# Performance work log

Hardware: AMD Instinct MI355X
Metric: run time of the kernel (lower is better)

Reference implementation:

```python
import jax, jax.numpy as jnp
import numpy as np
import math

B, S, D, H, DFF, L = 8, 1024, 512, 8, 2048, 4
DK = D // H
EPS = 1e-5
NEG = -1e32


def _sinusoidal_pe(s, d):
    pos = np.arange(s)[:, None].astype(np.float32)
    div = np.exp(np.arange(0, d, 2).astype(np.float32) * (-math.log(10000.0) / d))
    pe = np.zeros((s, d), np.float32)
    pe[:, 0::2] = np.sin(pos * div)
    pe[:, 1::2] = np.cos(pos * div)
    return jnp.asarray(pe)


def setup_inputs() -> dict:
    key = jax.random.key(0)
    ks = jax.random.split(key, 20)
    sd = 0.02
    inp = {
        "q_embed_data": jax.random.normal(ks[0], (B, S, D), jnp.float32),
        "qa_embed_data": jax.random.normal(ks[1], (B, S, D), jnp.float32),
        "pe": _sinusoidal_pe(S, D),
        # stacked per-layer params (leading dim L). kq_same=1 -> q uses Wk.
        "Wk": sd * jax.random.normal(ks[2], (L, D, D), jnp.float32),
        "bk": jnp.zeros((L, D), jnp.float32),
        "Wv": sd * jax.random.normal(ks[3], (L, D, D), jnp.float32),
        "bv": jnp.zeros((L, D), jnp.float32),
        "Wo": sd * jax.random.normal(ks[4], (L, D, D), jnp.float32),
        "bo": jnp.zeros((L, D), jnp.float32),
        "ln1_s": jnp.ones((L, D), jnp.float32),
        "ln1_b": jnp.zeros((L, D), jnp.float32),
        "W1": sd * jax.random.normal(ks[5], (L, D, DFF), jnp.float32),
        "b1": jnp.zeros((L, DFF), jnp.float32),
        "W2": sd * jax.random.normal(ks[6], (L, DFF, D), jnp.float32),
        "b2": jnp.zeros((L, D), jnp.float32),
        "ln2_s": jnp.ones((L, D), jnp.float32),
        "ln2_b": jnp.zeros((L, D), jnp.float32),
    }
    return inp


def _layernorm(z, s, b):
    m = z.mean(-1, keepdims=True)
    v = ((z - m) ** 2).mean(-1, keepdims=True)
    return (z - m) / jnp.sqrt(v + EPS) * s + b


def _forward(q_embed_data, qa_embed_data, pe, Wk, bk, Wv, bv, Wo, bo,
             ln1_s, ln1_b, W1, b1, W2, b2, ln2_s, ln2_b):
    x = q_embed_data + pe[None, :, :]
    y = qa_embed_data + pe[None, :, :]  # values source stays fixed across blocks
    allowed = jnp.tril(jnp.ones((S, S), bool), -1)  # strictly-causal: attend only to j < i
    row_keep = (jnp.arange(S) > 0).astype(x.dtype)[None, None, :, None]  # zero_pad row 0

    def heads(z, W, b):
        return (z @ W + b).reshape(B, S, H, DK).transpose(0, 2, 1, 3)  # [B,H,S,DK]

    def step(xc, p):
        wk, bk_, wv, bv_, wo, bo_, s1, b1n, w1, b1f, w2, b2f, s2, b2n = p
        q = heads(xc, wk, bk_)  # kq_same: q via k_linear
        k = heads(xc, wk, bk_)
        v = heads(y, wv, bv_)
        sc = jnp.einsum('bhid,bhjd->bhij', q, k) / math.sqrt(DK)
        att = jax.nn.softmax(jnp.where(allowed, sc, NEG), axis=-1) * row_keep
        o = jnp.einsum('bhij,bhjd->bhid', att, v).transpose(0, 2, 1, 3).reshape(B, S, D)
        x1 = _layernorm(xc + (o @ wo + bo_), s1, b1n)
        f = jax.nn.relu(x1 @ w1 + b1f) @ w2 + b2f
        x2 = _layernorm(x1 + f, s2, b2n)
        return x2, None

    out, _ = jax.lax.scan(step, x, (Wk, bk, Wv, bv, Wo, bo, ln1_s, ln1_b, W1, b1, W2, b2, ln2_s, ln2_b))
    return out


def reference(q_embed_data, qa_embed_data, pe, Wk, bk, Wv, bv, Wo, bo,
              ln1_s, ln1_b, W1, b1, W2, b2, ln2_s, ln2_b):
    return _forward(q_embed_data, qa_embed_data, pe, Wk, bk, Wv, bv, Wo, bo,
                    ln1_s, ln1_b, W1, b1, W2, b2, ln2_s, ln2_b)
```

## Files before the change

kernel.cpp:

```cpp
#include <hip/hip_runtime.h>
#include <stdint.h>

typedef __attribute__((ext_vector_type(8))) __bf16 bf16x8;
typedef __attribute__((ext_vector_type(4))) float f32x4;
typedef __attribute__((ext_vector_type(4))) unsigned int u32x4;

constexpr int B = 8, S = 1024, D = 512, H = 8, DFF = 2048, L = 4, DK = 64;
constexpr int MR = B * S;

__device__ __forceinline__ unsigned short f2bf(float f) {
    union { float f; unsigned u; } v; v.f = f;
    unsigned u = v.u;
    u += 0x7fffu + ((u >> 16) & 1u);
    return (unsigned short)(u >> 16);
}

__device__ __forceinline__ void gload_lds16(const void* g, void* l) {
    __builtin_amdgcn_global_load_lds(
        (const __attribute__((address_space(1))) void*)g,
        (__attribute__((address_space(3))) void*)l, 16, 0, 0);
}

__global__ __launch_bounds__(256) void add_pe_kernel(
    const float* __restrict__ qe, const float* __restrict__ qa,
    const float* __restrict__ pe, float* __restrict__ x_f32,
    unsigned short* __restrict__ x_bf, unsigned short* __restrict__ y_bf) {
    int gid = blockIdx.x * 256 + threadIdx.x;
    int base = gid * 4;
    int po = base & (S * D - 1);
    float4 p = *(const float4*)(pe + po);
    float4 a = *(const float4*)(qe + base);
    float4 q = *(const float4*)(qa + base);
    float4 xv = make_float4(a.x + p.x, a.y + p.y, a.z + p.z, a.w + p.w);
    float4 yv = make_float4(q.x + p.x, q.y + p.y, q.z + p.z, q.w + p.w);
    *(float4*)(x_f32 + base) = xv;
    ushort4 xb; xb.x = f2bf(xv.x); xb.y = f2bf(xv.y); xb.z = f2bf(xv.z); xb.w = f2bf(xv.w);
    ushort4 yb; yb.x = f2bf(yv.x); yb.y = f2bf(yv.y); yb.z = f2bf(yv.z); yb.w = f2bf(yv.w);
    *(ushort4*)(x_bf + base) = xb;
    *(ushort4*)(y_bf + base) = yb;
}

__global__ __launch_bounds__(256) void wtrans_kernel(
    const float* __restrict__ src, unsigned short* __restrict__ dst, int K, int N) {
    __shared__ float t[64][65];
    src += (size_t)blockIdx.z * K * N;
    dst += (size_t)blockIdx.z * K * N;
    int n0 = blockIdx.x * 64, k0 = blockIdx.y * 64;
    int tid = threadIdx.x;
    int r = tid >> 4, c4 = (tid & 15) * 4;
    #pragma unroll
    for (int rr = 0; rr < 64; rr += 16) {
        float4 v = *(const float4*)(src + (size_t)(k0 + r + rr) * N + n0 + c4);
        t[r + rr][c4] = v.x; t[r + rr][c4 + 1] = v.y;
        t[r + rr][c4 + 2] = v.z; t[r + rr][c4 + 3] = v.w;
    }
    __syncthreads();
    int n = tid >> 2, kc = (tid & 3) * 16;
    ushort4 o[4];
    #pragma unroll
    for (int g = 0; g < 4; g++) {
        o[g].x = f2bf(t[kc + g * 4 + 0][n]);
        o[g].y = f2bf(t[kc + g * 4 + 1][n]);
        o[g].z = f2bf(t[kc + g * 4 + 2][n]);
        o[g].w = f2bf(t[kc + g * 4 + 3][n]);
    }
    unsigned short* dp = dst + (size_t)(n0 + n) * K + k0 + kc;
    #pragma unroll
    for (int g = 0; g < 4; g++) *(ushort4*)(dp + g * 4) = o[g];
}

template<int BN, bool RELU, bool RESID, bool OUT_F32, bool OUT_BF16, bool OUT_VT>
__global__ __launch_bounds__(256) void gemm_kernel(
    const unsigned short* __restrict__ A, const unsigned short* __restrict__ Bt,
    const float* __restrict__ bias, const float* __restrict__ resid,
    float* __restrict__ out_f32, unsigned short* __restrict__ out_bf,
    int M, int N, int K) {
    constexpr int MT = (BN == 128) ? 4 : 2;
    constexpr int WROWS = (BN == 128) ? 64 : 32;
    constexpr int BRND = (BN == 128) ? 4 : 2;
    __shared__ unsigned short a_lds[128 * 64];
    __shared__ unsigned short b_lds[BN * 64];

    const int tid = threadIdx.x;
    const int lane = tid & 63, wid = tid >> 6;
    const int wm = (BN == 128) ? (wid >> 1) : wid;
    const int wn = (BN == 128) ? (wid & 1) : 0;
    const int l15 = lane & 15, quad = lane >> 4;
    const int nmt = gridDim.x, nnt = gridDim.y;
    const int o_lin = blockIdx.y * nmt + blockIdx.x;
    const int xcd = o_lin & 7, oi = o_lin >> 3;
    const int mtile = xcd * (nmt >> 3) + oi / nnt;
    const int ntile = oi % nnt;
    const int m0 = mtile * 128, n0 = ntile * BN;

    f32x4 acc[MT][4];
    #pragma unroll
    for (int i = 0; i < MT; i++)
        #pragma unroll
        for (int j = 0; j < 4; j++) { f32x4 z = {0.f, 0.f, 0.f, 0.f}; acc[i][j] = z; }

    const unsigned short* aP[4];
    unsigned short* aL[4];
    #pragma unroll
    for (int j = 0; j < 4; j++) {
        int c = wid * 256 + j * 64 + lane;
        int r = c >> 3, slot = c & 7, kg = slot ^ (r & 7);
        aP[j] = A + (size_t)(m0 + r) * K + kg * 8;
        aL[j] = a_lds + (size_t)(wid * 256 + j * 64) * 8;
    }
    const unsigned short* bP[BRND];
    unsigned short* bL[BRND];
    #pragma unroll
    for (int j = 0; j < BRND; j++) {
        int c = wid * (BRND * 64) + j * 64 + lane;
        int r = c >> 3, slot = c & 7, kg = slot ^ (r & 7);
        bP[j] = Bt + (size_t)(n0 + r) * K + kg * 8;
        bL[j] = b_lds + (size_t)(wid * (BRND * 64) + j * 64) * 8;
    }

    for (int k0 = 0; k0 < K; k0 += 64) {
        #pragma unroll
        for (int j = 0; j < 4; j++) gload_lds16(aP[j] + k0, aL[j]);
        #pragma unroll
        for (int j = 0; j < BRND; j++) gload_lds16(bP[j] + k0, bL[j]);
        __syncthreads();

        bf16x8 af[MT][2], bfv[4][2];
        #pragma unroll
        for (int mt = 0; mt < MT; mt++) {
            int row = wm * WROWS + mt * 16 + l15;
            #pragma unroll
            for (int kh = 0; kh < 2; kh++)
                af[mt][kh] = *(const bf16x8*)&a_lds[row * 64 + (((kh * 4 + quad) ^ (row & 7)) * 8)];
        }
        #pragma unroll
        for (int nt = 0; nt < 4; nt++) {
            int row = wn * 64 + nt * 16 + l15;
            #pragma unroll
            for (int kh = 0; kh < 2; kh++)
                bfv[nt][kh] = *(const bf16x8*)&b_lds[row * 64 + (((kh * 4 + quad) ^ (row & 7)) * 8)];
        }
        #pragma unroll
        for (int mt = 0; mt < MT; mt++)
            #pragma unroll
            for (int nt = 0; nt < 4; nt++) {
                acc[mt][nt] = __builtin_amdgcn_mfma_f32_16x16x32_bf16(af[mt][0], bfv[nt][0], acc[mt][nt], 0, 0, 0);
                acc[mt][nt] = __builtin_amdgcn_mfma_f32_16x16x32_bf16(af[mt][1], bfv[nt][1], acc[mt][nt], 0, 0, 0);
            }
        __syncthreads();
    }

    #pragma unroll
    for (int nt = 0; nt < 4; nt++) {
        int col = n0 + wn * 64 + nt * 16 + l15;
        float bv = bias[col];
        #pragma unroll
        for (int mt = 0; mt < MT; mt++) {
            int row0 = m0 + wm * WROWS + mt * 16 + quad * 4;
            if (OUT_VT) {
                int hh = col >> 6, d = col & 63;
                int bb = row0 >> 10, s0 = row0 & 1023;
                ushort4 o;
                o.x = f2bf(acc[mt][nt][0] + bv);
                o.y = f2bf(acc[mt][nt][1] + bv);
                o.z = f2bf(acc[mt][nt][2] + bv);
                o.w = f2bf(acc[mt][nt][3] + bv);
                *(ushort4*)(out_bf + ((size_t)(bb * H + hh) * DK + d) * S + s0) = o;
            } else {
                #pragma unroll
                for (int r = 0; r < 4; r++) {
                    int row = row0 + r;
                    float v = acc[mt][nt][r] + bv;
                    if (RESID) v += resid[(size_t)row * N + col];
                    if (RELU) v = fmaxf(v, 0.f);
                    size_t o = (size_t)row * N + col;
                    if (OUT_F32) out_f32[o] = v;
                    if (OUT_BF16) out_bf[o] = f2bf(v);
                }
            }
        }
    }
}

__global__ __launch_bounds__(256) void gemm_qkv_kernel(
    const unsigned short* __restrict__ x_bf, const unsigned short* __restrict__ y_bf,
    const unsigned short* __restrict__ wkT, const unsigned short* __restrict__ wvT,
    const float* __restrict__ bk, const float* __restrict__ bv,
    unsigned short* __restrict__ qk_out, unsigned short* __restrict__ vt_out) {
    constexpr int BN = 64, MT = 2, WROWS = 32, BRND = 2;
    constexpr int N = 512, K = 512;
    __shared__ unsigned short a_lds[128 * 64];
    __shared__ unsigned short b_lds[BN * 64];

    const bool isv = blockIdx.z != 0;
    const unsigned short* A  = isv ? y_bf : x_bf;
    const unsigned short* Bt = isv ? wvT : wkT;
    const float* bias        = isv ? bv : bk;

    const int tid = threadIdx.x;
    const int lane = tid & 63, wid = tid >> 6;
    const int l15 = lane & 15, quad = lane >> 4;
    const int nmt = gridDim.x, nnt = gridDim.y;
    const int o_lin = blockIdx.y * nmt + blockIdx.x;
    const int xcd = o_lin & 7, oi = o_lin >> 3;
    const int mtile = xcd * (nmt >> 3) + oi / nnt;
    const int ntile = oi % nnt;
    const int m0 = mtile * 128, n0 = ntile * BN;

    f32x4 acc[MT][4];
    #pragma unroll
    for (int i = 0; i < MT; i++)
        #pragma unroll
        for (int j = 0; j < 4; j++) { f32x4 z = {0.f, 0.f, 0.f, 0.f}; acc[i][j] = z; }

    const unsigned short* aP[4];
    unsigned short* aL[4];
    #pragma unroll
    for (int j = 0; j < 4; j++) {
        int c = wid * 256 + j * 64 + lane;
        int r = c >> 3, slot = c & 7, kg = slot ^ (r & 7);
        aP[j] = A + (size_t)(m0 + r) * K + kg * 8;
        aL[j] = a_lds + (size_t)(wid * 256 + j * 64) * 8;
    }
    const unsigned short* bP[BRND];
    unsigned short* bL[BRND];
    #pragma unroll
    for (int j = 0; j < BRND; j++) {
        int c = wid * (BRND * 64) + j * 64 + lane;
        int r = c >> 3, slot = c & 7, kg = slot ^ (r & 7);
        bP[j] = Bt + (size_t)(n0 + r) * K + kg * 8;
        bL[j] = b_lds + (size_t)(wid * (BRND * 64) + j * 64) * 8;
    }

    for (int k0 = 0; k0 < K; k0 += 64) {
        #pragma unroll
        for (int j = 0; j < 4; j++) gload_lds16(aP[j] + k0, aL[j]);
        #pragma unroll
        for (int j = 0; j < BRND; j++) gload_lds16(bP[j] + k0, bL[j]);
        __syncthreads();

        bf16x8 af[MT][2], bfv[4][2];
        #pragma unroll
        for (int mt = 0; mt < MT; mt++) {
            int row = wid * WROWS + mt * 16 + l15;
            #pragma unroll
            for (int kh = 0; kh < 2; kh++)
                af[mt][kh] = *(const bf16x8*)&a_lds[row * 64 + (((kh * 4 + quad) ^ (row & 7)) * 8)];
        }
        #pragma unroll
        for (int nt = 0; nt < 4; nt++) {
            int row = nt * 16 + l15;
            #pragma unroll
            for (int kh = 0; kh < 2; kh++)
                bfv[nt][kh] = *(const bf16x8*)&b_lds[row * 64 + (((kh * 4 + quad) ^ (row & 7)) * 8)];
        }
        #pragma unroll
        for (int mt = 0; mt < MT; mt++)
            #pragma unroll
            for (int nt = 0; nt < 4; nt++) {
                acc[mt][nt] = __builtin_amdgcn_mfma_f32_16x16x32_bf16(af[mt][0], bfv[nt][0], acc[mt][nt], 0, 0, 0);
                acc[mt][nt] = __builtin_amdgcn_mfma_f32_16x16x32_bf16(af[mt][1], bfv[nt][1], acc[mt][nt], 0, 0, 0);
            }
        __syncthreads();
    }

    #pragma unroll
    for (int nt = 0; nt < 4; nt++) {
        int col = n0 + nt * 16 + l15;
        float bv_ = bias[col];
        #pragma unroll
        for (int mt = 0; mt < MT; mt++) {
            int row0 = m0 + wid * WROWS + mt * 16 + quad * 4;
            ushort4 o;
            o.x = f2bf(acc[mt][nt][0] + bv_);
            o.y = f2bf(acc[mt][nt][1] + bv_);
            o.z = f2bf(acc[mt][nt][2] + bv_);
            o.w = f2bf(acc[mt][nt][3] + bv_);
            if (isv) {
                int hh = col >> 6, d = col & 63;
                int bb = row0 >> 10, s0 = row0 & 1023;
                *(ushort4*)(vt_out + ((size_t)(bb * H + hh) * DK + d) * S + s0) = o;
            } else {
                #pragma unroll
                for (int r = 0; r < 4; r++)
                    qk_out[(size_t)(row0 + r) * N + col] =
                        (r == 0) ? o.x : (r == 1) ? o.y : (r == 2) ? o.z : o.w;
            }
        }
    }
}

__global__ __launch_bounds__(256) void ln_kernel(
    const float* __restrict__ in, const float* __restrict__ gamma,
    const float* __restrict__ beta, float* __restrict__ out_f32,
    unsigned short* __restrict__ out_bf) {
    __shared__ float red[8];
    int row = blockIdx.x, tid = threadIdx.x;
    const float* p = in + (size_t)row * D;
    float2 v = *(const float2*)(p + tid * 2);
    float s = v.x + v.y;
    float q = v.x * v.x + v.y * v.y;
    #pragma unroll
    for (int off = 32; off > 0; off >>= 1) {
        s += __shfl_xor(s, off);
        q += __shfl_xor(q, off);
    }
    int wid = tid >> 6, lane = tid & 63;
    if (lane == 0) { red[wid] = s; red[4 + wid] = q; }
    __syncthreads();
    s = red[0] + red[1] + red[2] + red[3];
    q = red[4] + red[5] + red[6] + red[7];
    float mean = s * (1.f / D);
    float var = q * (1.f / D) - mean * mean;
    float inv = rsqrtf(var + 1e-5f);
    int c = tid * 2;
    float2 g = *(const float2*)(gamma + c);
    float2 bb = *(const float2*)(beta + c);
    float o0 = (v.x - mean) * inv * g.x + bb.x;
    float o1 = (v.y - mean) * inv * g.y + bb.y;
    *(float2*)(out_f32 + (size_t)row * D + c) = make_float2(o0, o1);
    ushort2 ob; ob.x = f2bf(o0); ob.y = f2bf(o1);
    *(ushort2*)(out_bf + (size_t)row * D + c) = ob;
}

__global__ __launch_bounds__(256, 2) void attn_kernel(
    const unsigned short* __restrict__ qk, const unsigned short* __restrict__ vt,
    unsigned short* __restrict__ ob) {
    __shared__ unsigned short kbuf[2][64 * 64];
    __shared__ unsigned short vbuf[2][64 * 64];
    __shared__ unsigned p_u32[4][32 * 36];
    constexpr float C = 0.18033688011112042f;
    const float NEGINF = -__builtin_huge_valf();

    const int bx = blockIdx.x;
    const int Qb = 7 - (bx >> 6);
    const int hh = bx & 63;
    const int b = hh >> 3, h = hh & 7;
    const int head = hh;
    const int tid = threadIdx.x;
    const int w = tid >> 6, lane = tid & 63;
    const int l15 = lane & 15, quad = lane >> 4;

    const int nkt = 2 * Qb + 2;
    const int qrow0 = Qb * 128 + w * 32;

    const int rowbase = b * S, colbase = h * DK;
    const unsigned short* kbase = qk + (size_t)rowbase * D + colbase;
    const unsigned short* vbase = vt + (size_t)head * (DK * S);

    bf16x8 qf[2][2];
    #pragma unroll
    for (int u = 0; u < 2; u++) {
        const unsigned short* qrow =
            qk + (size_t)(rowbase + qrow0 + u * 16 + l15) * D + colbase;
        qf[u][0] = *(const bf16x8*)(qrow + quad * 8);
        qf[u][1] = *(const bf16x8*)(qrow + 32 + quad * 8);
    }

    const int sr = lane >> 3;
    const int sseg = (lane & 7) ^ sr;
    const unsigned short* kgp[2]; const unsigned short* vgp[2];
    unsigned short* kld[2]; unsigned short* vld[2];
    #pragma unroll
    for (int j = 0; j < 2; j++) {
        int rt = w * 16 + j * 8 + sr;
        kgp[j] = kbase + (size_t)rt * D + sseg * 8;
        vgp[j] = vbase + (size_t)rt * S + sseg * 8;
        kld[j] = &kbuf[0][(w * 16 + j * 8) * 64];
        vld[j] = &vbuf[0][(w * 16 + j * 8) * 64];
    }
    auto stage = [&](int buf, int kt) {
        #pragma unroll
        for (int j = 0; j < 2; j++) gload_lds16(kgp[j] + (size_t)kt * 64 * D, kld[j] + buf * 4096);
        #pragma unroll
        for (int j = 0; j < 2; j++) gload_lds16(vgp[j] + kt * 64, vld[j] + buf * 4096);
    };

    float l_r[2] = {0.f, 0.f};
    f32x4 o_acc[2][4];
    #pragma unroll
    for (int u = 0; u < 2; u++)
        #pragma unroll
        for (int i = 0; i < 4; i++) { f32x4 z = {0.f, 0.f, 0.f, 0.f}; o_acc[u][i] = z; }

    auto consume = [&](int kt, const unsigned short* kl, const unsigned short* vl) {
        unsigned* pb = p_u32[w];
        bf16x8 kf[4][2];
        #pragma unroll
        for (int mt = 0; mt < 4; mt++) {
            const unsigned short* kr = kl + (mt * 16 + l15) * 64;
            #pragma unroll
            for (int kh = 0; kh < 2; kh++)
                kf[mt][kh] = *(const bf16x8*)(kr + (((kh * 4 + quad) ^ (l15 & 7)) * 8));
        }
        const bool diag = kt * 64 + 64 > qrow0;
        #pragma unroll
        for (int u = 0; u < 2; u++) {
            const int qb = qrow0 + u * 16;
            const int ql = u * 16 + l15;
            #pragma unroll
            for (int mt = 0; mt < 4; mt++) {
                if (kt * 64 + mt * 16 < qb + 16) {
                    f32x4 a = {0.f, 0.f, 0.f, 0.f};
                    a = __builtin_amdgcn_mfma_f32_16x16x32_bf16(kf[mt][0], qf[u][0], a, 0, 0, 0);
                    a = __builtin_amdgcn_mfma_f32_16x16x32_bf16(kf[mt][1], qf[u][1], a, 0, 0, 0);
                    if (diag) {
                        const int gi = qb + l15;
                        #pragma unroll
                        for (int r = 0; r < 4; r++) {
                            int gj = kt * 64 + mt * 16 + quad * 4 + r;
                            a[r] = (gj >= gi) ? NEGINF : a[r];
                        }
                    }
                    float e0 = exp2f(a[0] * C), e1 = exp2f(a[1] * C);
                    float e2 = exp2f(a[2] * C), e3 = exp2f(a[3] * C);
                    unsigned pk0, pk1;
                    asm("v_cvt_pk_bf16_f32 %0, %1, %2" : "=v"(pk0) : "v"(e0), "v"(e1));
                    asm("v_cvt_pk_bf16_f32 %0, %1, %2" : "=v"(pk1) : "v"(e2), "v"(e3));
                    l_r[u] += (e0 + e1) + (e2 + e3);
                    *(uint2*)&pb[ql * 36 + mt * 8 + quad * 2] = make_uint2(pk0, pk1);
                } else {
                    *(uint2*)&pb[ql * 36 + mt * 8 + quad * 2] = make_uint2(0u, 0u);
                }
            }
        }
        bf16x8 vf[4][2];
        #pragma unroll
        for (int mt = 0; mt < 4; mt++) {
            const unsigned short* vr = vl + (mt * 16 + l15) * 64;
            #pragma unroll
            for (int kh = 0; kh < 2; kh++)
                vf[mt][kh] = *(const bf16x8*)(vr + (((kh * 4 + quad) ^ (l15 & 7)) * 8));
        }
        #pragma unroll
        for (int u = 0; u < 2; u++) {
            const int qb = qrow0 + u * 16;
            const int ql = u * 16 + l15;
            u32x4 d0 = *(const u32x4*)&pb[ql * 36 + quad * 4];
            bf16x8 pb0 = __builtin_bit_cast(bf16x8, d0);
            const bool hi = (kt * 64 + 32 < qb + 16);
            if (hi) {
                u32x4 d1 = *(const u32x4*)&pb[ql * 36 + 16 + quad * 4];
                bf16x8 pb1 = __builtin_bit_cast(bf16x8, d1);
                #pragma unroll
                for (int mt = 0; mt < 4; mt++) {
                    o_acc[u][mt] = __builtin_amdgcn_mfma_f32_16x16x32_bf16(vf[mt][0], pb0, o_acc[u][mt], 0, 0, 0);
                    o_acc[u][mt] = __builtin_amdgcn_mfma_f32_16x16x32_bf16(vf[mt][1], pb1, o_acc[u][mt], 0, 0, 0);
                }
            } else {
                #pragma unroll
                for (int mt = 0; mt < 4; mt++)
                    o_acc[u][mt] = __builtin_amdgcn_mfma_f32_16x16x32_bf16(vf[mt][0], pb0, o_acc[u][mt], 0, 0, 0);
            }
        }
    };

    stage(0, 0);
    for (int kt = 0; kt < nkt; ++kt) {
        const int cur = kt & 1;
        if (kt + 1 < nkt) {
            stage(cur ^ 1, kt + 1);
            asm volatile("s_waitcnt vmcnt(4)" ::: "memory");
        } else {
            asm volatile("s_waitcnt vmcnt(0)" ::: "memory");
        }
        __builtin_amdgcn_sched_barrier(0);
        __builtin_amdgcn_s_barrier();
        __builtin_amdgcn_sched_barrier(0);
        if (kt * 64 < qrow0 + 32)
            consume(kt, &kbuf[cur][0], &vbuf[cur][0]);
        __builtin_amdgcn_sched_barrier(0);
        __builtin_amdgcn_s_barrier();
        __builtin_amdgcn_sched_barrier(0);
    }

    #pragma unroll
    for (int u = 0; u < 2; u++) {
        l_r[u] += __shfl_xor(l_r[u], 16);
        l_r[u] += __shfl_xor(l_r[u], 32);
    }
    #pragma unroll
    for (int u = 0; u < 2; u++) {
        const int si = qrow0 + u * 16 + l15;
        float inv = (l_r[u] > 0.f) ? 1.f / l_r[u] : 0.f;
        if (si == 0) inv = 0.f;
        unsigned short* orow = ob + (size_t)(b * S + si) * D + h * DK;
        #pragma unroll
        for (int mt = 0; mt < 4; mt++) {
            ushort4 o;
            o.x = f2bf(o_acc[u][mt][0] * inv);
            o.y = f2bf(o_acc[u][mt][1] * inv);
            o.z = f2bf(o_acc[u][mt][2] * inv);
            o.w = f2bf(o_acc[u][mt][3] * inv);
            *(ushort4*)(orow + mt * 16 + quad * 4) = o;
        }
    }
}

extern "C" void kernel_launch(void* const* d_in, const int* in_sizes, int n_in,
                              void* d_out, int out_size, void* d_ws, size_t ws_size,
                              hipStream_t stream) {
    (void)in_sizes; (void)n_in; (void)out_size; (void)ws_size;
    const float* qe  = (const float*)d_in[0];
    const float* qa  = (const float*)d_in[1];
    const float* pe  = (const float*)d_in[2];
    const float* Wk  = (const float*)d_in[3];
    const float* bk  = (const float*)d_in[4];
    const float* Wv  = (const float*)d_in[5];
    const float* bv  = (const float*)d_in[6];
    const float* Wo  = (const float*)d_in[7];
    const float* bo  = (const float*)d_in[8];
    const float* l1s = (const float*)d_in[9];
    const float* l1b = (const float*)d_in[10];
    const float* W1  = (const float*)d_in[11];
    const float* b1  = (const float*)d_in[12];
    const float* W2  = (const float*)d_in[13];
    const float* b2  = (const float*)d_in[14];
    const float* l2s = (const float*)d_in[15];
    const float* l2b = (const float*)d_in[16];

    char* w = (char*)d_ws;
    float* x_f32  = (float*)w;           w += (size_t)MR * D * 4;
    float* t_f32  = (float*)w;           w += (size_t)MR * D * 4;
    float* x1_f32 = (float*)w;           w += (size_t)MR * D * 4;
    unsigned short* x_bf  = (unsigned short*)w; w += (size_t)MR * D * 2;
    unsigned short* y_bf  = (unsigned short*)w; w += (size_t)MR * D * 2;
    unsigned short* qk_bf = (unsigned short*)w; w += (size_t)MR * D * 2;
    unsigned short* vt_bf = (unsigned short*)w; w += (size_t)MR * D * 2;
    unsigned short* o_bf  = (unsigned short*)w; w += (size_t)MR * D * 2;
    unsigned short* x1_bf = (unsigned short*)w; w += (size_t)MR * D * 2;
    unsigned short* h_bf  = (unsigned short*)w; w += (size_t)MR * DFF * 2;
    unsigned short* wkT = (unsigned short*)w;   w += (size_t)L * D * D * 2;
    unsigned short* wvT = (unsigned short*)w;   w += (size_t)L * D * D * 2;
    unsigned short* woT = (unsigned short*)w;   w += (size_t)L * D * D * 2;
    unsigned short* w1T = (unsigned short*)w;   w += (size_t)L * D * DFF * 2;
    unsigned short* w2T = (unsigned short*)w;   w += (size_t)L * DFF * D * 2;

    add_pe_kernel<<<MR * D / 4 / 256, 256, 0, stream>>>(qe, qa, pe, x_f32, x_bf, y_bf);
    wtrans_kernel<<<dim3(8, 8, L), 256, 0, stream>>>(Wk, wkT, D, D);
    wtrans_kernel<<<dim3(8, 8, L), 256, 0, stream>>>(Wv, wvT, D, D);
    wtrans_kernel<<<dim3(8, 8, L), 256, 0, stream>>>(Wo, woT, D, D);
    wtrans_kernel<<<dim3(32, 8, L), 256, 0, stream>>>(W1, w1T, D, DFF);
    wtrans_kernel<<<dim3(8, 32, L), 256, 0, stream>>>(W2, w2T, DFF, D);

    dim3 g512(64, 8), g2048(64, 16);
    for (int l = 0; l < L; l++) {
        gemm_qkv_kernel<<<dim3(64, 8, 2), 256, 0, stream>>>(
            x_bf, y_bf, wkT + (size_t)l * D * D, wvT + (size_t)l * D * D,
            bk + l * D, bv + l * D, qk_bf, vt_bf);
        attn_kernel<<<512, 256, 0, stream>>>(qk_bf, vt_bf, o_bf);
        gemm_kernel<64, false, true, true, false, false><<<g512, 256, 0, stream>>>(
            o_bf, woT + (size_t)l * D * D, bo + l * D, x_f32, t_f32, nullptr, MR, D, D);
        ln_kernel<<<MR, 256, 0, stream>>>(t_f32, l1s + l * D, l1b + l * D, x1_f32, x1_bf);
        gemm_kernel<128, true, false, false, true, false><<<g2048, 256, 0, stream>>>(
            x1_bf, w1T + (size_t)l * D * DFF, b1 + l * DFF, nullptr, nullptr, h_bf, MR, DFF, D);
        gemm_kernel<64, false, true, true, false, false><<<g512, 256, 0, stream>>>(
            h_bf, w2T + (size_t)l * DFF * D, b2 + l * D, x1_f32, t_f32, nullptr, MR, D, DFF);
        float* xo = (l == L - 1) ? (float*)d_out : x_f32;
        ln_kernel<<<MR, 256, 0, stream>>>(t_f32, l2s + l * D, l2b + l * D, xo, x_bf);
    }
}
```

Measured before the change: 718.6 us.

## Double-buffer LDS tiles in GEMM kernels to overlap global loads with MFMA

Both the generic GEMM and the fused QKV GEMM now use two LDS buffers per operand and prefetch the next K-tile while the current one is computed. Partial s_waitcnt vmcnt counts let the next tile's loads stay in flight across the barrier. The aim is to hide global-to-LDS latency behind MFMA work. In exchange LDS use per block doubles, which may reduce occupancy, and the hand-written waitcnt counts must exactly match the number of issued loads.

```diff
diff --git a/kernel.cpp b/kernel.cpp
--- a/kernel.cpp
+++ b/kernel.cpp
@@ -78,8 +78,8 @@
     constexpr int MT = (BN == 128) ? 4 : 2;
     constexpr int WROWS = (BN == 128) ? 64 : 32;
     constexpr int BRND = (BN == 128) ? 4 : 2;
-    __shared__ unsigned short a_lds[128 * 64];
-    __shared__ unsigned short b_lds[BN * 64];
+    __shared__ unsigned short a_lds[2][128 * 64];
+    __shared__ unsigned short b_lds[2][BN * 64];
 
     const int tid = threadIdx.x;
     const int lane = tid & 63, wid = tid >> 6;
@@ -106,7 +106,7 @@
         int c = wid * 256 + j * 64 + lane;
         int r = c >> 3, slot = c & 7, kg = slot ^ (r & 7);
         aP[j] = A + (size_t)(m0 + r) * K + kg * 8;
-        aL[j] = a_lds + (size_t)(wid * 256 + j * 64) * 8;
+        aL[j] = &a_lds[0][(size_t)(wid * 256 + j * 64) * 8];
     }
     const unsigned short* bP[BRND];
     unsigned short* bL[BRND];
@@ -115,15 +115,29 @@
         int c = wid * (BRND * 64) + j * 64 + lane;
         int r = c >> 3, slot = c & 7, kg = slot ^ (r & 7);
         bP[j] = Bt + (size_t)(n0 + r) * K + kg * 8;
-        bL[j] = b_lds + (size_t)(wid * (BRND * 64) + j * 64) * 8;
-    }
-
-    for (int k0 = 0; k0 < K; k0 += 64) {
-        #pragma unroll
-        for (int j = 0; j < 4; j++) gload_lds16(aP[j] + k0, aL[j]);
-        #pragma unroll
-        for (int j = 0; j < BRND; j++) gload_lds16(bP[j] + k0, bL[j]);
-        __syncthreads();
+        bL[j] = &b_lds[0][(size_t)(wid * (BRND * 64) + j * 64) * 8];
+    }
+
+    auto stage = [&](int buf, int k0) {
+        #pragma unroll
+        for (int j = 0; j < 4; j++) gload_lds16(aP[j] + k0, aL[j] + buf * (128 * 64));
+        #pragma unroll
+        for (int j = 0; j < BRND; j++) gload_lds16(bP[j] + k0, bL[j] + buf * (BN * 64));
+    };
+
+    stage(0, 0);
+    for (int k0 = 0, st = 0; k0 < K; k0 += 64, ++st) {
+        const int cur = st & 1;
+        if (k0 + 64 < K) {
+            stage(cur ^ 1, k0 + 64);
+            if constexpr (BN == 128) asm volatile("s_waitcnt vmcnt(8)" ::: "memory");
+            else                     asm volatile("s_waitcnt vmcnt(6)" ::: "memory");
+        } else {
+            asm volatile("s_waitcnt vmcnt(0)" ::: "memory");
+        }
+        __builtin_amdgcn_sched_barrier(0);
+        __builtin_amdgcn_s_barrier();
+        __builtin_amdgcn_sched_barrier(0);
 
         bf16x8 af[MT][2], bfv[4][2];
         #pragma unroll
@@ -131,14 +145,14 @@
             int row = wm * WROWS + mt * 16 + l15;
             #pragma unroll
             for (int kh = 0; kh < 2; kh++)
-                af[mt][kh] = *(const bf16x8*)&a_lds[row * 64 + (((kh * 4 + quad) ^ (row & 7)) * 8)];
+                af[mt][kh] = *(const bf16x8*)&a_lds[cur][row * 64 + (((kh * 4 + quad) ^ (row & 7)) * 8)];
         }
         #pragma unroll
         for (int nt = 0; nt < 4; nt++) {
             int row = wn * 64 + nt * 16 + l15;
             #pragma unroll
             for (int kh = 0; kh < 2; kh++)
-                bfv[nt][kh] = *(const bf16x8*)&b_lds[row * 64 + (((kh * 4 + quad) ^ (row & 7)) * 8)];
+                bfv[nt][kh] = *(const bf16x8*)&b_lds[cur][row * 64 + (((kh * 4 + quad) ^ (row & 7)) * 8)];
         }
         #pragma unroll
         for (int mt = 0; mt < MT; mt++)
@@ -147,7 +161,9 @@
                 acc[mt][nt] = __builtin_amdgcn_mfma_f32_16x16x32_bf16(af[mt][0], bfv[nt][0], acc[mt][nt], 0, 0, 0);
                 acc[mt][nt] = __builtin_amdgcn_mfma_f32_16x16x32_bf16(af[mt][1], bfv[nt][1], acc[mt][nt], 0, 0, 0);
             }
-        __syncthreads();
+        __builtin_amdgcn_sched_barrier(0);
+        __builtin_amdgcn_s_barrier();
+        __builtin_amdgcn_sched_barrier(0);
     }
 
     #pragma unroll
@@ -189,8 +205,8 @@
     unsigned short* __restrict__ qk_out, unsigned short* __restrict__ vt_out) {
     constexpr int BN = 64, MT = 2, WROWS = 32, BRND = 2;
     constexpr int N = 512, K = 512;
-    __shared__ unsigned short a_lds[128 * 64];
-    __shared__ unsigned short b_lds[BN * 64];
+    __shared__ unsigned short a_lds[2][128 * 64];
+    __shared__ unsigned short b_lds[2][BN * 64];
 
     const bool isv = blockIdx.z != 0;
     const unsigned short* A  = isv ? y_bf : x_bf;
@@ -220,7 +236,7 @@
         int c = wid * 256 + j * 64 + lane;
         int r = c >> 3, slot = c & 7, kg = slot ^ (r & 7);
         aP[j] = A + (size_t)(m0 + r) * K + kg * 8;
-        aL[j] = a_lds + (size_t)(wid * 256 + j * 64) * 8;
+        aL[j] = &a_lds[0][(size_t)(wid * 256 + j * 64) * 8];
     }
     const unsigned short* bP[BRND];
     unsigned short* bL[BRND];
@@ -229,15 +245,28 @@
         int c = wid * (BRND * 64) + j * 64 + lane;
         int r = c >> 3, slot = c & 7, kg = slot ^ (r & 7);
         bP[j] = Bt + (size_t)(n0 + r) * K + kg * 8;
-        bL[j] = b_lds + (size_t)(wid * (BRND * 64) + j * 64) * 8;
-    }
-
-    for (int k0 = 0; k0 < K; k0 += 64) {
-        #pragma unroll
-        for (int j = 0; j < 4; j++) gload_lds16(aP[j] + k0, aL[j]);
-        #pragma unroll
-        for (int j = 0; j < BRND; j++) gload_lds16(bP[j] + k0, bL[j]);
-        __syncthreads();
+        bL[j] = &b_lds[0][(size_t)(wid * (BRND * 64) + j * 64) * 8];
+    }
+
+    auto stage = [&](int buf, int k0) {
+        #pragma unroll
+        for (int j = 0; j < 4; j++) gload_lds16(aP[j] + k0, aL[j] + buf * (128 * 64));
+        #pragma unroll
+        for (int j = 0; j < BRND; j++) gload_lds16(bP[j] + k0, bL[j] + buf * (BN * 64));
+    };
+
+    stage(0, 0);
+    for (int k0 = 0, st = 0; k0 < K; k0 += 64, ++st) {
+        const int cur = st & 1;
+        if (k0 + 64 < K) {
+            stage(cur ^ 1, k0 + 64);
+            asm volatile("s_waitcnt vmcnt(6)" ::: "memory");
+        } else {
+            asm volatile("s_waitcnt vmcnt(0)" ::: "memory");
+        }
+        __builtin_amdgcn_sched_barrier(0);
+        __builtin_amdgcn_s_barrier();
+        __builtin_amdgcn_sched_barrier(0);
 
         bf16x8 af[MT][2], bfv[4][2];
         #pragma unroll
@@ -245,14 +274,14 @@
             int row = wid * WROWS + mt * 16 + l15;
             #pragma unroll
             for (int kh = 0; kh < 2; kh++)
-                af[mt][kh] = *(const bf16x8*)&a_lds[row * 64 + (((kh * 4 + quad) ^ (row & 7)) * 8)];
+                af[mt][kh] = *(const bf16x8*)&a_lds[cur][row * 64 + (((kh * 4 + quad) ^ (row & 7)) * 8)];
         }
         #pragma unroll
         for (int nt = 0; nt < 4; nt++) {
             int row = nt * 16 + l15;
             #pragma unroll
             for (int kh = 0; kh < 2; kh++)
-                bfv[nt][kh] = *(const bf16x8*)&b_lds[row * 64 + (((kh * 4 + quad) ^ (row & 7)) * 8)];
+                bfv[nt][kh] = *(const bf16x8*)&b_lds[cur][row * 64 + (((kh * 4 + quad) ^ (row & 7)) * 8)];
         }
         #pragma unroll
         for (int mt = 0; mt < MT; mt++)
@@ -261,7 +290,9 @@
                 acc[mt][nt] = __builtin_amdgcn_mfma_f32_16x16x32_bf16(af[mt][0], bfv[nt][0], acc[mt][nt], 0, 0, 0);
                 acc[mt][nt] = __builtin_amdgcn_mfma_f32_16x16x32_bf16(af[mt][1], bfv[nt][1], acc[mt][nt], 0, 0, 0);
             }
-        __syncthreads();
+        __builtin_amdgcn_sched_barrier(0);
+        __builtin_amdgcn_s_barrier();
+        __builtin_amdgcn_sched_barrier(0);
     }
 
     #pragma unroll
```

New measurement: 718.8 us. Within noise of the previous version (+0.0%).

## Stage GEMM epilogue through LDS for vector stores; hoist V projection out of layer loop

Applied to the files above, without the earlier changes.

The GEMM epilogue now writes the accumulators into a per-wave LDS scratch area and reads them back row-contiguous, so bias, residual and outputs move as float4 or 16-byte vectors instead of scattered scalar accesses. Because the value source y never changes across layers, the V projections for all four layers are computed in one launch before the loop and kept in a larger buffer, leaving only the Q/K GEMM inside each layer. This removes poorly coalesced epilogue traffic and the per-layer V work on the critical path. In exchange it uses extra LDS round trips and a wider workspace for the per-layer V tensors.

```diff
diff --git a/kernel.cpp b/kernel.cpp
--- a/kernel.cpp
+++ b/kernel.cpp
@@ -69,7 +69,7 @@
     for (int g = 0; g < 4; g++) *(ushort4*)(dp + g * 4) = o[g];
 }
 
-template<int BN, bool RELU, bool RESID, bool OUT_F32, bool OUT_BF16, bool OUT_VT>
+template<int BN, bool RELU, bool RESID, bool OUT_F32, bool OUT_BF16>
 __global__ __launch_bounds__(256) void gemm_kernel(
     const unsigned short* __restrict__ A, const unsigned short* __restrict__ Bt,
     const float* __restrict__ bias, const float* __restrict__ resid,
@@ -78,8 +78,9 @@
     constexpr int MT = (BN == 128) ? 4 : 2;
     constexpr int WROWS = (BN == 128) ? 64 : 32;
     constexpr int BRND = (BN == 128) ? 4 : 2;
-    __shared__ unsigned short a_lds[128 * 64];
-    __shared__ unsigned short b_lds[BN * 64];
+    __shared__ unsigned short lds[(128 + BN) * 64];
+    unsigned short* a_lds = lds;
+    unsigned short* b_lds = lds + 128 * 64;
 
     const int tid = threadIdx.x;
     const int lane = tid & 63, wid = tid >> 6;
@@ -150,52 +151,71 @@
         __syncthreads();
     }
 
-    #pragma unroll
-    for (int nt = 0; nt < 4; nt++) {
-        int col = n0 + wn * 64 + nt * 16 + l15;
-        float bv = bias[col];
-        #pragma unroll
-        for (int mt = 0; mt < MT; mt++) {
-            int row0 = m0 + wm * WROWS + mt * 16 + quad * 4;
-            if (OUT_VT) {
-                int hh = col >> 6, d = col & 63;
-                int bb = row0 >> 10, s0 = row0 & 1023;
-                ushort4 o;
-                o.x = f2bf(acc[mt][nt][0] + bv);
-                o.y = f2bf(acc[mt][nt][1] + bv);
-                o.z = f2bf(acc[mt][nt][2] + bv);
-                o.w = f2bf(acc[mt][nt][3] + bv);
-                *(ushort4*)(out_bf + ((size_t)(bb * H + hh) * DK + d) * S + s0) = o;
-            } else {
-                #pragma unroll
-                for (int r = 0; r < 4; r++) {
-                    int row = row0 + r;
-                    float v = acc[mt][nt][r] + bv;
-                    if (RESID) v += resid[(size_t)row * N + col];
-                    if (RELU) v = fmaxf(v, 0.f);
-                    size_t o = (size_t)row * N + col;
-                    if (OUT_F32) out_f32[o] = v;
-                    if (OUT_BF16) out_bf[o] = f2bf(v);
-                }
+    float* sc = (float*)lds + wid * (16 * 68);
+    const int cbase = n0 + wn * 64;
+    const int r2 = lane >> 2;
+    const int c2 = (lane & 3) * 16;
+    float4 bvv[4];
+    #pragma unroll
+    for (int i = 0; i < 4; i++) bvv[i] = *(const float4*)(bias + cbase + c2 + i * 4);
+    #pragma unroll
+    for (int mt = 0; mt < MT; mt++) {
+        #pragma unroll
+        for (int nt = 0; nt < 4; nt++)
+            #pragma unroll
+            for (int r = 0; r < 4; r++)
+                sc[(quad * 4 + r) * 68 + nt * 16 + l15] = acc[mt][nt][r];
+        const int row_g = m0 + wm * WROWS + mt * 16 + r2;
+        float v[16];
+        #pragma unroll
+        for (int i = 0; i < 4; i++) {
+            float4 t = *(const float4*)&sc[r2 * 68 + c2 + i * 4];
+            v[i * 4 + 0] = t.x + bvv[i].x; v[i * 4 + 1] = t.y + bvv[i].y;
+            v[i * 4 + 2] = t.z + bvv[i].z; v[i * 4 + 3] = t.w + bvv[i].w;
+        }
+        if (RESID) {
+            const float* rp = resid + (size_t)row_g * N + cbase + c2;
+            #pragma unroll
+            for (int i = 0; i < 4; i++) {
+                float4 t = *(const float4*)(rp + i * 4);
+                v[i * 4 + 0] += t.x; v[i * 4 + 1] += t.y;
+                v[i * 4 + 2] += t.z; v[i * 4 + 3] += t.w;
             }
         }
-    }
-}
-
-__global__ __launch_bounds__(256) void gemm_qkv_kernel(
-    const unsigned short* __restrict__ x_bf, const unsigned short* __restrict__ y_bf,
-    const unsigned short* __restrict__ wkT, const unsigned short* __restrict__ wvT,
-    const float* __restrict__ bk, const float* __restrict__ bv,
-    unsigned short* __restrict__ qk_out, unsigned short* __restrict__ vt_out) {
-    constexpr int BN = 64, MT = 2, WROWS = 32, BRND = 2;
+        if (RELU) {
+            #pragma unroll
+            for (int i = 0; i < 16; i++) v[i] = fmaxf(v[i], 0.f);
+        }
+        if (OUT_F32) {
+            float* op = out_f32 + (size_t)row_g * N + cbase + c2;
+            #pragma unroll
+            for (int i = 0; i < 4; i++)
+                *(float4*)(op + i * 4) = make_float4(v[i * 4], v[i * 4 + 1], v[i * 4 + 2], v[i * 4 + 3]);
+        }
+        if (OUT_BF16) {
+            unsigned short ob[16];
+            #pragma unroll
+            for (int i = 0; i < 16; i++) ob[i] = f2bf(v[i]);
+            unsigned short* op = out_bf + (size_t)row_g * N + cbase + c2;
+            *(u32x4*)op = *(const u32x4*)ob;
+            *(u32x4*)(op + 8) = *(const u32x4*)(ob + 8);
+        }
+    }
+}
+
+__global__ __launch_bounds__(256) void gemm_vt_kernel(
+    const unsigned short* __restrict__ y_bf, const unsigned short* __restrict__ wvT_all,
+    const float* __restrict__ bv_all, unsigned short* __restrict__ vt_all) {
+    constexpr int BN = 64, MT = 2, BRND = 2;
     constexpr int N = 512, K = 512;
-    __shared__ unsigned short a_lds[128 * 64];
-    __shared__ unsigned short b_lds[BN * 64];
-
-    const bool isv = blockIdx.z != 0;
-    const unsigned short* A  = isv ? y_bf : x_bf;
-    const unsigned short* Bt = isv ? wvT : wkT;
-    const float* bias        = isv ? bv : bk;
+    __shared__ unsigned short lds[(128 + BN) * 64];
+    unsigned short* a_lds = lds;
+    unsigned short* b_lds = lds + 128 * 64;
+
+    const int lyr = blockIdx.z;
+    const unsigned short* Bt = wvT_all + (size_t)lyr * D * D;
+    const float* bias = bv_all + (size_t)lyr * D;
+    unsigned short* vt_out = vt_all + (size_t)lyr * MR * D;
 
     const int tid = threadIdx.x;
     const int lane = tid & 63, wid = tid >> 6;
@@ -219,7 +239,7 @@
     for (int j = 0; j < 4; j++) {
         int c = wid * 256 + j * 64 + lane;
         int r = c >> 3, slot = c & 7, kg = slot ^ (r & 7);
-        aP[j] = A + (size_t)(m0 + r) * K + kg * 8;
+        aP[j] = y_bf + (size_t)(m0 + r) * K + kg * 8;
         aL[j] = a_lds + (size_t)(wid * 256 + j * 64) * 8;
     }
     const unsigned short* bP[BRND];
@@ -242,7 +262,7 @@
         bf16x8 af[MT][2], bfv[4][2];
         #pragma unroll
         for (int mt = 0; mt < MT; mt++) {
-            int row = wid * WROWS + mt * 16 + l15;
+            int row = wid * 32 + mt * 16 + l15;
             #pragma unroll
             for (int kh = 0; kh < 2; kh++)
                 af[mt][kh] = *(const bf16x8*)&a_lds[row * 64 + (((kh * 4 + quad) ^ (row & 7)) * 8)];
@@ -270,22 +290,15 @@
         float bv_ = bias[col];
         #pragma unroll
         for (int mt = 0; mt < MT; mt++) {
-            int row0 = m0 + wid * WROWS + mt * 16 + quad * 4;
+            int row0 = m0 + wid * 32 + mt * 16 + quad * 4;
             ushort4 o;
             o.x = f2bf(acc[mt][nt][0] + bv_);
             o.y = f2bf(acc[mt][nt][1] + bv_);
             o.z = f2bf(acc[mt][nt][2] + bv_);
             o.w = f2bf(acc[mt][nt][3] + bv_);
-            if (isv) {
-                int hh = col >> 6, d = col & 63;
-                int bb = row0 >> 10, s0 = row0 & 1023;
-                *(ushort4*)(vt_out + ((size_t)(bb * H + hh) * DK + d) * S + s0) = o;
-            } else {
-                #pragma unroll
-                for (int r = 0; r < 4; r++)
-                    qk_out[(size_t)(row0 + r) * N + col] =
-                        (r == 0) ? o.x : (r == 1) ? o.y : (r == 2) ? o.z : o.w;
-            }
+            int hh = col >> 6, d = col & 63;
+            int bb = row0 >> 10, s0 = row0 & 1023;
+            *(ushort4*)(vt_out + ((size_t)(bb * H + hh) * DK + d) * S + s0) = o;
         }
     }
 }
@@ -526,10 +539,10 @@
     unsigned short* x_bf  = (unsigned short*)w; w += (size_t)MR * D * 2;
     unsigned short* y_bf  = (unsigned short*)w; w += (size_t)MR * D * 2;
     unsigned short* qk_bf = (unsigned short*)w; w += (size_t)MR * D * 2;
-    unsigned short* vt_bf = (unsigned short*)w; w += (size_t)MR * D * 2;
     unsigned short* o_bf  = (unsigned short*)w; w += (size_t)MR * D * 2;
     unsigned short* x1_bf = (unsigned short*)w; w += (size_t)MR * D * 2;
     unsigned short* h_bf  = (unsigned short*)w; w += (size_t)MR * DFF * 2;
+    unsigned short* vt_bf = (unsigned short*)w; w += (size_t)L * MR * D * 2;
     unsigned short* wkT = (unsigned short*)w;   w += (size_t)L * D * D * 2;
     unsigned short* wvT = (unsigned short*)w;   w += (size_t)L * D * D * 2;
     unsigned short* woT = (unsigned short*)w;   w += (size_t)L * D * D * 2;
@@ -542,19 +555,19 @@
     wtrans_kernel<<<dim3(8, 8, L), 256, 0, stream>>>(Wo, woT, D, D);
     wtrans_kernel<<<dim3(32, 8, L), 256, 0, stream>>>(W1, w1T, D, DFF);
     wtrans_kernel<<<dim3(8, 32, L), 256, 0, stream>>>(W2, w2T, DFF, D);
+    gemm_vt_kernel<<<dim3(64, 8, L), 256, 0, stream>>>(y_bf, wvT, bv, vt_bf);
 
     dim3 g512(64, 8), g2048(64, 16);
     for (int l = 0; l < L; l++) {
-        gemm_qkv_kernel<<<dim3(64, 8, 2), 256, 0, stream>>>(
-            x_bf, y_bf, wkT + (size_t)l * D * D, wvT + (size_t)l * D * D,
-            bk + l * D, bv + l * D, qk_bf, vt_bf);
-        attn_kernel<<<512, 256, 0, stream>>>(qk_bf, vt_bf, o_bf);
-        gemm_kernel<64, false, true, true, false, false><<<g512, 256, 0, stream>>>(
+        gemm_kernel<64, false, false, false, true><<<g512, 256, 0, stream>>>(
+            x_bf, wkT + (size_t)l * D * D, bk + l * D, nullptr, nullptr, qk_bf, MR, D, D);
+        attn_kernel<<<512, 256, 0, stream>>>(qk_bf, vt_bf + (size_t)l * MR * D, o_bf);
+        gemm_kernel<64, false, true, true, false><<<g512, 256, 0, stream>>>(
             o_bf, woT + (size_t)l * D * D, bo + l * D, x_f32, t_f32, nullptr, MR, D, D);
         ln_kernel<<<MR, 256, 0, stream>>>(t_f32, l1s + l * D, l1b + l * D, x1_f32, x1_bf);
-        gemm_kernel<128, true, false, false, true, false><<<g2048, 256, 0, stream>>>(
+        gemm_kernel<128, true, false, false, true><<<g2048, 256, 0, stream>>>(
             x1_bf, w1T + (size_t)l * D * DFF, b1 + l * DFF, nullptr, nullptr, h_bf, MR, DFF, D);
-        gemm_kernel<64, false, true, true, false, false><<<g512, 256, 0, stream>>>(
+        gemm_kernel<64, false, true, true, false><<<g512, 256, 0, stream>>>(
             h_bf, w2T + (size_t)l * DFF * D, b2 + l * D, x1_f32, t_f32, nullptr, MR, D, DFF);
         float* xo = (l == L - 1) ? (float*)d_out : x_f32;
         ln_kernel<<<MR, 256, 0, stream>>>(t_f32, l2s + l * D, l2b + l * D, xo, x_bf);
```

Result: slower. 746.5 us (+3.9%).
